# Kernel tuning notes

Measured on AMD Instinct MI355X. Metric: run time of the kernel, lower is better.

## Reference

```python
import jax, jax.numpy as jnp
import numpy as np

BLOCK = 16           # NVFP4 block size along in_features
E2M1_MAX = 6.0       # max representable FP4 E2M1 magnitude
E4M3_MAX = 448.0     # max representable FP8 E4M3 magnitude
_TINY = 1e-30


def _quant_e2m1(x):
    """Round to nearest FP4 E2M1 value {0, +-0.5, 1, 1.5, 2, 3, 4, 6} (RNE)."""
    s = jnp.sign(x)
    ax = jnp.clip(jnp.abs(x), 0.0, E2M1_MAX)
    e = jnp.clip(jnp.floor(jnp.log2(jnp.maximum(ax, _TINY))), 0.0, 2.0)
    step = jnp.exp2(e)  # spacing within this binade is step/2 (1 mantissa bit)
    q = jnp.round(ax / step * 2.0) / 2.0 * step  # jnp.round = half-to-even
    return s * q


def _quant_e4m3(x):
    """Round to nearest FP8 E4M3 value (3 mantissa bits, subnormal min 2^-9)."""
    s = jnp.sign(x)
    ax = jnp.clip(jnp.abs(x), 0.0, E4M3_MAX)
    e = jnp.clip(jnp.floor(jnp.log2(jnp.maximum(ax, _TINY))), -6.0, 8.0)
    step = jnp.exp2(e)
    q = jnp.round(ax / step * 8.0) / 8.0 * step
    return s * q


def nvfp4_dequant_weight(weight, per_block_amax, global_amax):
    O, I = weight.shape
    nb = I // BLOCK
    # two-level scale: global fp32 scale + per-block E4M3 scale
    gscale = global_amax / (E2M1_MAX * E4M3_MAX)                 # scalar
    blk_scale_f = per_block_amax / E2M1_MAX                      # [O, nb]
    blk_scale = _quant_e4m3(blk_scale_f / gscale) * gscale       # [O, nb]
    wb = weight.reshape(O, nb, BLOCK)
    sb = blk_scale[:, :, None]
    wq = jnp.where(sb > 0, wb / jnp.maximum(sb, _TINY), 0.0)
    w_dq = _quant_e2m1(wq) * sb
    return w_dq.reshape(O, I)


def setup_inputs() -> dict:
    key = jax.random.key(0)
    kx, kw = jax.random.split(key)
    O, I, T = 4096, 4096, 8192
    x = jax.random.normal(kx, (T, I), dtype=jnp.float32)
    weight = jax.random.normal(kw, (O, I), dtype=jnp.float32)
    # amax values derived from the weight (static calibration)
    per_block_amax = jnp.max(jnp.abs(weight.reshape(O, I // BLOCK, BLOCK)), axis=-1)
    global_amax = jnp.max(jnp.abs(weight))
    return {"x": x, "weight": weight, "per_block_amax": per_block_amax,
            "global_amax": global_amax}


def reference(x, weight, per_block_amax, global_amax):
    w_dq = nvfp4_dequant_weight(weight, per_block_amax, global_amax)
    return jnp.matmul(x, w_dq.T)  # [T, O]
```

## Files before the change

### kernel.cpp

```cpp
#include <hip/hip_runtime.h>

typedef unsigned short u16;
typedef unsigned int u32;
typedef __attribute__((ext_vector_type(8))) __bf16 bf16x8;
typedef __attribute__((ext_vector_type(8))) unsigned short ushort8;
typedef __attribute__((ext_vector_type(4))) float f32x4;

__device__ __forceinline__ u16 f32_to_bf16(float f) {
  u32 u = __float_as_uint(f);
  u = (u + 0x7fffu + ((u >> 16) & 1u)) >> 16;
  return (u16)u;
}

__global__ void cvt_x_bf16(const float* __restrict__ x, u16* __restrict__ o, long n8) {
  long i = (long)blockIdx.x * blockDim.x + threadIdx.x;
  if (i >= n8) return;
  const float4* p = (const float4*)x + i * 2;
  float4 a = p[0], b = p[1];
  ushort8 v;
  v[0] = f32_to_bf16(a.x); v[1] = f32_to_bf16(a.y);
  v[2] = f32_to_bf16(a.z); v[3] = f32_to_bf16(a.w);
  v[4] = f32_to_bf16(b.x); v[5] = f32_to_bf16(b.y);
  v[6] = f32_to_bf16(b.z); v[7] = f32_to_bf16(b.w);
  *(ushort8*)(o + i * 8) = v;
}

__global__ void dequant_w(const float* __restrict__ w, const float* __restrict__ pba,
                          const float* __restrict__ gp, u16* __restrict__ wq, int nblk) {
  int i = blockIdx.x * blockDim.x + threadIdx.x;
  if (i >= nblk) return;
  float g = *gp;
  float gscale = g / 2688.0f;
  float ratio = (pba[i] / 6.0f) / gscale;
  ratio = fminf(fmaxf(ratio, 0.0f), 448.0f);
  int e = (int)((__float_as_uint(ratio) >> 23) & 0xffu) - 127;
  if (e < -6) e = -6;
  float stp = __uint_as_float((u32)(e - 3 + 127) << 23);
  float e4 = rintf(ratio / stp) * stp;
  float sb = e4 * gscale;
  float den = fmaxf(sb, 1e-30f);
  bool pos = sb > 0.0f;

  const float4* wp = (const float4*)(w + (size_t)i * 16);
  float vals[16];
#pragma unroll
  for (int t = 0; t < 4; ++t) {
    float4 v = wp[t];
    vals[4 * t + 0] = v.x; vals[4 * t + 1] = v.y;
    vals[4 * t + 2] = v.z; vals[4 * t + 3] = v.w;
  }
  ushort8 o0, o1;
#pragma unroll
  for (int k = 0; k < 16; ++k) {
    float wv = pos ? vals[k] / den : 0.0f;
    float s = (wv < 0.0f) ? -1.0f : 1.0f;
    float ax = fminf(fabsf(wv), 6.0f);
    float h = ax < 2.0f ? 0.5f : (ax < 4.0f ? 1.0f : 2.0f);
    float q = rintf(ax / h) * h;
    u16 r = f32_to_bf16(s * q * e4);
    if (k < 8) o0[k] = r; else o1[k - 8] = r;
  }
  ushort8* dst = (ushort8*)(wq + (size_t)i * 16);
  dst[0] = o0; dst[1] = o1;
}

#define GLL16(gp_, lp_)                                              \
  __builtin_amdgcn_global_load_lds(                                  \
      (__attribute__((address_space(1))) void*)(gp_),                \
      (__attribute__((address_space(3))) void*)(lp_), 16, 0, 0)

__global__ __launch_bounds__(256) void gemm_bt(
    const u16* __restrict__ A, const u16* __restrict__ B,
    float* __restrict__ C, const float* __restrict__ gp,
    int M, int N, int K) {
  __shared__ u16 sA[128 * 32];
  __shared__ u16 sB[128 * 32];
  const int tid = threadIdx.x;
  const int lane = tid & 63;
  const int wave = tid >> 6;
  const int m0 = blockIdx.y * 128;
  const int n0 = blockIdx.x * 128;

  f32x4 zero = {0.0f, 0.0f, 0.0f, 0.0f};
  f32x4 acc[4][4];
#pragma unroll
  for (int i = 0; i < 4; ++i)
#pragma unroll
    for (int j = 0; j < 4; ++j) acc[i][j] = zero;

  const int srow = wave * 32 + (lane >> 2);
  const int scol = (lane & 3) * 8;
  const u16* gA = A + (size_t)(m0 + srow) * K + scol;
  const u16* gB = B + (size_t)(n0 + srow) * K + scol;
  u16* lA0 = &sA[(wave * 32) * 32];
  u16* lA1 = &sA[(wave * 32 + 16) * 32];
  u16* lB0 = &sB[(wave * 32) * 32];
  u16* lB1 = &sB[(wave * 32 + 16) * 32];
  const size_t rstep = (size_t)16 * K;

  const int fr = lane & 15;
  const int fq = (lane >> 4) * 8;
  const int wm = (wave >> 1) * 64;
  const int wn = (wave & 1) * 64;

  for (int k0 = 0; k0 < K; k0 += 32) {
    __syncthreads();
    GLL16(gA + k0, lA0);
    GLL16(gA + k0 + rstep, lA1);
    GLL16(gB + k0, lB0);
    GLL16(gB + k0 + rstep, lB1);
    __syncthreads();

    bf16x8 af[4], bfr[4];
#pragma unroll
    for (int i = 0; i < 4; ++i)
      af[i] = *(const bf16x8*)&sA[(wm + i * 16 + fr) * 32 + fq];
#pragma unroll
    for (int j = 0; j < 4; ++j)
      bfr[j] = *(const bf16x8*)&sB[(wn + j * 16 + fr) * 32 + fq];
#pragma unroll
    for (int i = 0; i < 4; ++i)
#pragma unroll
      for (int j = 0; j < 4; ++j)
        acc[i][j] = __builtin_amdgcn_mfma_f32_16x16x32_bf16(af[i], bfr[j], acc[i][j], 0, 0, 0);
  }

  const float gs = (*gp) / 2688.0f;
  const int crow = m0 + wm + (lane >> 4) * 4;
  const int ccol = n0 + wn + (lane & 15);
#pragma unroll
  for (int i = 0; i < 4; ++i)
#pragma unroll
    for (int r = 0; r < 4; ++r) {
      float* cp = C + (size_t)(crow + i * 16 + r) * N + ccol;
#pragma unroll
      for (int j = 0; j < 4; ++j)
        cp[j * 16] = acc[i][j][r] * gs;
    }
}

extern "C" void kernel_launch(void* const* d_in, const int* in_sizes, int n_in,
                              void* d_out, int out_size, void* d_ws, size_t ws_size,
                              hipStream_t stream) {
  const float* x   = (const float*)d_in[0];
  const float* w   = (const float*)d_in[1];
  const float* pba = (const float*)d_in[2];
  const float* gam = (const float*)d_in[3];
  float* out = (float*)d_out;

  const int T = 8192, I = 4096, O = 4096;
  u16* xb = (u16*)d_ws;
  u16* wb = xb + (size_t)T * I;

  long n8 = (long)T * I / 8;
  hipLaunchKernelGGL(cvt_x_bf16, dim3((unsigned)((n8 + 255) / 256)), dim3(256), 0, stream,
                     x, xb, n8);
  int nblk = O * (I / 16);
  hipLaunchKernelGGL(dequant_w, dim3(nblk / 256), dim3(256), 0, stream,
                     w, pba, gam, wb, nblk);
  hipLaunchKernelGGL(gemm_bt, dim3(O / 128, T / 128), dim3(256), 0, stream,
                     xb, wb, out, gam, T, O, I);
}
```

Before: 620.1 us.

## Rewrite GEMM as 256x256 tile with 4-stage async LDS pipeline and swizzle

Result: faster. 522.3 us (-15.8%).

```diff
diff --git a/kernel.cpp b/kernel.cpp
--- a/kernel.cpp
+++ b/kernel.cpp
@@ -69,73 +69,132 @@
       (__attribute__((address_space(1))) void*)(gp_),                \
       (__attribute__((address_space(3))) void*)(lp_), 16, 0, 0)
 
-__global__ __launch_bounds__(256) void gemm_bt(
+#define SBAR()                                   \
+  do {                                           \
+    __builtin_amdgcn_sched_barrier(0);           \
+    __builtin_amdgcn_s_barrier();                \
+    __builtin_amdgcn_sched_barrier(0);           \
+  } while (0)
+
+template <int VM, bool STG>
+__device__ __forceinline__ void ktile(int t, u16 (&lds)[4][2][8192],
+                                      const u16* gAs, const u16* gBs, size_t rh,
+                                      int aro, int bro, int col8, int wave,
+                                      f32x4 (&acc)[8][4]) {
+  const u16* aL = &lds[t & 3][0][0];
+  const u16* bL = &lds[t & 3][1][0];
+  bf16x8 af[4], bv[4];
+  if (STG) {
+    u16* sd = &lds[(t + 3) & 3][0][wave * 512];
+    const u16* g = gAs + (size_t)(t + 3) * 32;
+    GLL16(g, sd);
+    GLL16(g + rh, sd + 4096);
+  }
+#pragma unroll
+  for (int m = 0; m < 4; ++m)
+    af[m] = *(const bf16x8*)&aL[(aro + m * 16) * 32 + col8];
+#pragma unroll
+  for (int n = 0; n < 4; ++n)
+    bv[n] = *(const bf16x8*)&bL[(bro + n * 16) * 32 + col8];
+  SBAR();
+  __builtin_amdgcn_s_setprio(1);
+#pragma unroll
+  for (int m = 0; m < 4; ++m)
+#pragma unroll
+    for (int n = 0; n < 4; ++n)
+      acc[m][n] = __builtin_amdgcn_mfma_f32_16x16x32_bf16(af[m], bv[n], acc[m][n], 0, 0, 0);
+  __builtin_amdgcn_s_setprio(0);
+  SBAR();
+  if (STG) {
+    u16* sd = &lds[(t + 3) & 3][1][wave * 512];
+    const u16* g = gBs + (size_t)(t + 3) * 32;
+    GLL16(g, sd);
+    GLL16(g + rh, sd + 4096);
+  }
+#pragma unroll
+  for (int m = 0; m < 4; ++m)
+    af[m] = *(const bf16x8*)&aL[(aro + 64 + m * 16) * 32 + col8];
+  asm volatile("s_waitcnt vmcnt(%0)" ::"n"(VM) : "memory");
+  SBAR();
+  __builtin_amdgcn_s_setprio(1);
+#pragma unroll
+  for (int m = 0; m < 4; ++m)
+#pragma unroll
+    for (int n = 0; n < 4; ++n)
+      acc[m + 4][n] =
+          __builtin_amdgcn_mfma_f32_16x16x32_bf16(af[m], bv[n], acc[m + 4][n], 0, 0, 0);
+  __builtin_amdgcn_s_setprio(0);
+  SBAR();
+}
+
+__global__ __launch_bounds__(512, 2) void gemm_bt(
     const u16* __restrict__ A, const u16* __restrict__ B,
     float* __restrict__ C, const float* __restrict__ gp,
     int M, int N, int K) {
-  __shared__ u16 sA[128 * 32];
-  __shared__ u16 sB[128 * 32];
+  __shared__ u16 lds[4][2][8192];
   const int tid = threadIdx.x;
   const int lane = tid & 63;
   const int wave = tid >> 6;
-  const int m0 = blockIdx.y * 128;
-  const int n0 = blockIdx.x * 128;
+
+  const int bid = blockIdx.x;
+  const int wg = (bid & 7) * 64 + (bid >> 3);
+  const int bx = wg >> 5;
+  const int by = wg & 31;
+  const int m0 = by * 256;
+  const int n0 = bx * 256;
+  const int NK = K >> 5;
 
   f32x4 zero = {0.0f, 0.0f, 0.0f, 0.0f};
-  f32x4 acc[4][4];
-#pragma unroll
-  for (int i = 0; i < 4; ++i)
+  f32x4 acc[8][4];
+#pragma unroll
+  for (int i = 0; i < 8; ++i)
 #pragma unroll
     for (int j = 0; j < 4; ++j) acc[i][j] = zero;
 
-  const int srow = wave * 32 + (lane >> 2);
-  const int scol = (lane & 3) * 8;
-  const u16* gA = A + (size_t)(m0 + srow) * K + scol;
-  const u16* gB = B + (size_t)(n0 + srow) * K + scol;
-  u16* lA0 = &sA[(wave * 32) * 32];
-  u16* lA1 = &sA[(wave * 32 + 16) * 32];
-  u16* lB0 = &sB[(wave * 32) * 32];
-  u16* lB1 = &sB[(wave * 32 + 16) * 32];
-  const size_t rstep = (size_t)16 * K;
-
-  const int fr = lane & 15;
-  const int fq = (lane >> 4) * 8;
-  const int wm = (wave >> 1) * 64;
-  const int wn = (wave & 1) * 64;
-
-  for (int k0 = 0; k0 < K; k0 += 32) {
-    __syncthreads();
-    GLL16(gA + k0, lA0);
-    GLL16(gA + k0 + rstep, lA1);
-    GLL16(gB + k0, lB0);
-    GLL16(gB + k0 + rstep, lB1);
-    __syncthreads();
-
-    bf16x8 af[4], bfr[4];
-#pragma unroll
-    for (int i = 0; i < 4; ++i)
-      af[i] = *(const bf16x8*)&sA[(wm + i * 16 + fr) * 32 + fq];
-#pragma unroll
-    for (int j = 0; j < 4; ++j)
-      bfr[j] = *(const bf16x8*)&sB[(wn + j * 16 + fr) * 32 + fq];
-#pragma unroll
-    for (int i = 0; i < 4; ++i)
-#pragma unroll
-      for (int j = 0; j < 4; ++j)
-        acc[i][j] = __builtin_amdgcn_mfma_f32_16x16x32_bf16(af[i], bfr[j], acc[i][j], 0, 0, 0);
-  }
+  const int wrow = wave >> 2;
+  const int wcol = wave & 3;
+
+  const int srow = wave * 16 + (lane >> 2);
+  const int scol = (((lane & 3) ^ ((lane >> 2) & 3)) << 3);
+  const u16* gAs = A + (size_t)(m0 + srow) * K + scol;
+  const u16* gBs = B + (size_t)(n0 + srow) * K + scol;
+  const size_t rh = (size_t)128 * K;
+
+  const int aro = wrow * 128 + (lane & 15);
+  const int bro = wcol * 64 + (lane & 15);
+  const int col8 = (((lane >> 4) ^ (lane & 3)) << 3);
+
+#pragma unroll
+  for (int t = 0; t < 3; ++t) {
+    u16* dA = &lds[t][0][wave * 512];
+    u16* dB = &lds[t][1][wave * 512];
+    const u16* ga = gAs + (size_t)t * 32;
+    const u16* gb = gBs + (size_t)t * 32;
+    GLL16(ga, dA);
+    GLL16(ga + rh, dA + 4096);
+    GLL16(gb, dB);
+    GLL16(gb + rh, dB + 4096);
+  }
+  asm volatile("s_waitcnt vmcnt(8)" ::: "memory");
+  SBAR();
+
+  int t = 0;
+  for (; t < NK - 3; ++t)
+    ktile<8, true>(t, lds, gAs, gBs, rh, aro, bro, col8, wave, acc);
+  ktile<4, false>(t, lds, gAs, gBs, rh, aro, bro, col8, wave, acc); ++t;
+  ktile<0, false>(t, lds, gAs, gBs, rh, aro, bro, col8, wave, acc); ++t;
+  ktile<0, false>(t, lds, gAs, gBs, rh, aro, bro, col8, wave, acc);
 
   const float gs = (*gp) / 2688.0f;
-  const int crow = m0 + wm + (lane >> 4) * 4;
-  const int ccol = n0 + wn + (lane & 15);
-#pragma unroll
-  for (int i = 0; i < 4; ++i)
+  const int crow = m0 + wrow * 128 + ((lane >> 4) << 2);
+  const int ccol = n0 + wcol * 64 + (lane & 15);
+#pragma unroll
+  for (int m = 0; m < 8; ++m)
 #pragma unroll
     for (int r = 0; r < 4; ++r) {
-      float* cp = C + (size_t)(crow + i * 16 + r) * N + ccol;
-#pragma unroll
-      for (int j = 0; j < 4; ++j)
-        cp[j * 16] = acc[i][j][r] * gs;
+      float* cp = C + (size_t)(crow + m * 16 + r) * N + ccol;
+#pragma unroll
+      for (int n = 0; n < 4; ++n) cp[n * 16] = acc[m][n][r] * gs;
     }
 }
 
@@ -158,6 +217,6 @@
   int nblk = O * (I / 16);
   hipLaunchKernelGGL(dequant_w, dim3(nblk / 256), dim3(256), 0, stream,
                      w, pba, gam, wb, nblk);
-  hipLaunchKernelGGL(gemm_bt, dim3(O / 128, T / 128), dim3(256), 0, stream,
+  hipLaunchKernelGGL(gemm_bt, dim3((O / 256) * (T / 256)), dim3(512), 0, stream,
                      xb, wb, out, gam, T, O, I);
 }
```
